# Kernel optimization log

Hardware: AMD Instinct MI355X
Metric: run time of the kernel (lower is better)

Reference implementation:

```python
import jax, jax.numpy as jnp
import numpy as np
import math

B, S, D = 4, 4096, 1024
H, HD, LK = 16, 64, 256


def setup_inputs() -> dict:
    key = jax.random.key(0)
    ks = jax.random.split(key, 8)
    s = 1.0 / math.sqrt(D)
    return {
        "X": jax.random.normal(ks[0], (B, S, D), jnp.float32),
        "mask": jnp.ones((B, S), jnp.float32),
        "Wq": jax.random.normal(ks[1], (D, H * HD), jnp.float32) * s,
        "bq": jnp.zeros((H * HD,), jnp.float32),
        "Wk": jax.random.normal(ks[2], (D, H * HD), jnp.float32) * s,
        "bk": jnp.zeros((H * HD,), jnp.float32),
        "Wv": jax.random.normal(ks[3], (D, H * HD), jnp.float32) * s,
        "bv": jnp.zeros((H * HD,), jnp.float32),
        "E": jax.random.normal(ks[4], (H, LK, S), jnp.float32) / math.sqrt(LK),
        "Wo": jax.random.normal(ks[5], (H * HD, D), jnp.float32) * s,
        "bo": jnp.zeros((D,), jnp.float32),
    }


def reference(X, mask, Wq, bq, Wk, bk, Wv, bv, E, Wo, bo):
    Bd, Sd, Dd = X.shape

    def split_heads(t):  # [B,S,H*HD] -> [B,H,S,HD]
        return t.reshape(Bd, Sd, H, HD).transpose(0, 2, 1, 3)

    Q = split_heads(X @ Wq + bq)
    K = split_heads(X @ Wk + bk)
    V = split_heads(X @ Wv + bv)

    m = mask[:, None, :, None]  # [B,1,S,1]
    # Low-rank projection along sequence: [H,LK,S] x [B,H,S,HD] -> [B,H,LK,HD]
    Kp = jnp.einsum('hks,bhsd->bhkd', E, K * m)
    Vp = jnp.einsum('hks,bhsd->bhkd', E, V * m)

    dot = jnp.einsum('bhsd,bhkd->bhsk', Q, Kp) / math.sqrt(HD)
    attn = jax.nn.softmax(dot, axis=-1)
    Xo = jnp.einsum('bhsk,bhkd->bhsd', attn, Vp)

    Xo = Xo.transpose(0, 2, 1, 3).reshape(Bd, Sd, H * HD)
    return Xo @ Wo + bo
```

## Files before the change

kernel.cpp:

```cpp
#include <hip/hip_runtime.h>
#include <hip/hip_bf16.h>
#include <stdint.h>

typedef __bf16 bf16_t;
typedef __attribute__((ext_vector_type(8))) __bf16 bf16x8;
typedef __attribute__((ext_vector_type(4))) __bf16 bf16x4;
typedef __attribute__((ext_vector_type(4))) float f32x4;

#define TO_GLB(p) ((const __attribute__((address_space(1))) void*)(p))
#define TO_LDS(p) ((__attribute__((address_space(3))) void*)(p))

__global__ __launch_bounds__(256) void cast_bf16_kernel(const float* __restrict__ src,
                                                        bf16_t* __restrict__ dst, int n4) {
  int i = blockIdx.x * 256 + threadIdx.x;
  if (i < n4) {
    float4 v = ((const float4*)src)[i];
    bf16x4 o;
    o[0] = (bf16_t)v.x; o[1] = (bf16_t)v.y; o[2] = (bf16_t)v.z; o[3] = (bf16_t)v.w;
    ((bf16x4*)dst)[i] = o;
  }
}

__global__ __launch_bounds__(256) void transpose_cast(const float* __restrict__ W,
                                                      bf16_t* __restrict__ out, int R, int C) {
  __shared__ bf16_t tile[64][72];
  int r0 = blockIdx.y * 64, c0 = blockIdx.x * 64;
  int tid = threadIdx.x;
#pragma unroll
  for (int p = 0; p < 4; ++p) {
    int r = p * 16 + (tid >> 4);
    int c = (tid & 15) * 4;
    float4 v = *(const float4*)(W + (size_t)(r0 + r) * C + c0 + c);
    tile[r][c + 0] = (bf16_t)v.x; tile[r][c + 1] = (bf16_t)v.y;
    tile[r][c + 2] = (bf16_t)v.z; tile[r][c + 3] = (bf16_t)v.w;
  }
  __syncthreads();
#pragma unroll
  for (int p = 0; p < 4; ++p) {
    int c = p * 16 + (tid >> 4);
    int r = (tid & 15) * 4;
    bf16x4 o;
    o[0] = tile[r + 0][c]; o[1] = tile[r + 1][c];
    o[2] = tile[r + 2][c]; o[3] = tile[r + 3][c];
    *(bf16x4*)(out + (size_t)(c0 + c) * R + r0 + r) = o;
  }
}

__global__ __launch_bounds__(256) void gemm_bt_128(
    const bf16_t* __restrict__ A, const bf16_t* __restrict__ B, int K, int mode,
    const float* __restrict__ bq, const float* __restrict__ bk, const float* __restrict__ bv,
    const float* __restrict__ mask,
    bf16_t* __restrict__ Q, bf16_t* __restrict__ KT, bf16_t* __restrict__ VT,
    const float* __restrict__ bo, float* __restrict__ out) {
  int tid = threadIdx.x;
  int lane = tid & 63, wv = tid >> 6;
  int wm = wv >> 1, wn = wv & 1;
  int q = lane >> 4, m_in = lane & 15;
  size_t m0 = (size_t)blockIdx.x * 128;
  size_t n0 = (size_t)blockIdx.y * 128;
  const bf16_t* Ab = A + m0 * K;
  const bf16_t* Bb = B + n0 * K;
  __shared__ __align__(16) bf16_t As[128 * 32];
  __shared__ __align__(16) bf16_t Bs[128 * 32];

  f32x4 acc[4][4];
  f32x4 z = {0.f, 0.f, 0.f, 0.f};
#pragma unroll
  for (int mt = 0; mt < 4; ++mt)
#pragma unroll
    for (int nt = 0; nt < 4; ++nt) acc[mt][nt] = z;

  for (int k0 = 0; k0 < K; k0 += 32) {
#pragma unroll
    for (int i = 0; i < 2; ++i) {
      int ch = wv * 128 + i * 64 + lane;
      const bf16_t* ga = Ab + (size_t)(ch >> 2) * K + k0 + (ch & 3) * 8;
      __builtin_amdgcn_global_load_lds(TO_GLB(ga), TO_LDS(As + (wv * 2 + i) * 512), 16, 0, 0);
      const bf16_t* gb = Bb + (size_t)(ch >> 2) * K + k0 + (ch & 3) * 8;
      __builtin_amdgcn_global_load_lds(TO_GLB(gb), TO_LDS(Bs + (wv * 2 + i) * 512), 16, 0, 0);
    }
    __syncthreads();
    bf16x8 af[4], bfr[4];
#pragma unroll
    for (int t = 0; t < 4; ++t)
      af[t] = *(const bf16x8*)(As + (wm * 64 + t * 16 + m_in) * 32 + q * 8);
#pragma unroll
    for (int t = 0; t < 4; ++t)
      bfr[t] = *(const bf16x8*)(Bs + (wn * 64 + t * 16 + m_in) * 32 + q * 8);
#pragma unroll
    for (int mt = 0; mt < 4; ++mt)
#pragma unroll
      for (int nt = 0; nt < 4; ++nt)
        acc[mt][nt] = __builtin_amdgcn_mfma_f32_16x16x32_bf16(af[mt], bfr[nt], acc[mt][nt], 0, 0, 0);
    __syncthreads();
  }

  if (mode == 0) {
#pragma unroll
    for (int mt = 0; mt < 4; ++mt) {
      int mbase = (int)m0 + wm * 64 + mt * 16 + q * 4;
      int b = mbase >> 12, s = mbase & 4095;
      float mk[4];
#pragma unroll
      for (int r = 0; r < 4; ++r) mk[r] = mask[b * 4096 + s + r];
#pragma unroll
      for (int nt = 0; nt < 4; ++nt) {
        int nG = (int)n0 + wn * 64 + nt * 16 + m_in;
        int proj = nG >> 10, c = nG & 1023, h = c >> 6, hd = c & 63;
        const float* bp = (proj == 0) ? bq : ((proj == 1) ? bk : bv);
        float bias = bp[c];
        if (proj == 0) {
#pragma unroll
          for (int r = 0; r < 4; ++r)
            Q[((size_t)(b * 16 + h) * 4096 + s + r) * 64 + hd] = (bf16_t)(acc[mt][nt][r] + bias);
        } else {
          bf16_t* dst = (proj == 1) ? KT : VT;
          bf16x4 v;
#pragma unroll
          for (int r = 0; r < 4; ++r) v[r] = (bf16_t)((acc[mt][nt][r] + bias) * mk[r]);
          *(bf16x4*)(dst + ((size_t)(b * 16 + h) * 64 + hd) * 4096 + s) = v;
        }
      }
    }
  } else {
#pragma unroll
    for (int mt = 0; mt < 4; ++mt) {
      int t = (int)m0 + wm * 64 + mt * 16 + q * 4;
#pragma unroll
      for (int nt = 0; nt < 4; ++nt) {
        int nG = (int)n0 + wn * 64 + nt * 16 + m_in;
        float bias = bo[nG];
#pragma unroll
        for (int r = 0; r < 4; ++r) out[(size_t)(t + r) * 1024 + nG] = acc[mt][nt][r] + bias;
      }
    }
  }
}

__global__ __launch_bounds__(512) void gemm2_kernel(
    const bf16_t* __restrict__ E, const bf16_t* __restrict__ KT, const bf16_t* __restrict__ VT,
    bf16_t* __restrict__ Kp, bf16_t* __restrict__ VpT) {
  int tid = threadIdx.x, lane = tid & 63, wv = tid >> 6;
  int wm = wv >> 1, wn = wv & 1;
  int q = lane >> 4, m_in = lane & 15;
  int mt0 = blockIdx.x;
  int bh = blockIdx.y;
  int kv = blockIdx.z;
  int h = bh & 15;
  const bf16_t* Ab = E + (size_t)h * 256 * 4096 + (size_t)mt0 * 128 * 4096;
  const bf16_t* Bb = (kv ? VT : KT) + (size_t)bh * 64 * 4096;
  __shared__ __align__(16) bf16_t As[4 * 128 * 32];
  __shared__ __align__(16) bf16_t Bs[4 * 64 * 32];

  f32x4 acc[2][2];
  f32x4 z = {0.f, 0.f, 0.f, 0.f};
#pragma unroll
  for (int mt = 0; mt < 2; ++mt)
#pragma unroll
    for (int nt = 0; nt < 2; ++nt) acc[mt][nt] = z;

  for (int k0 = 0; k0 < 4096; k0 += 128) {
#pragma unroll
    for (int it = 0; it < 4; ++it) {
      int l = it * 512 + tid;
      int sub = l >> 9, row = (l >> 2) & 127, cc = l & 3;
      const bf16_t* ga = Ab + (size_t)row * 4096 + k0 + sub * 32 + cc * 8;
      __builtin_amdgcn_global_load_lds(TO_GLB(ga), TO_LDS(As + (it * 512 + wv * 64) * 8), 16, 0, 0);
    }
#pragma unroll
    for (int it = 0; it < 2; ++it) {
      int l = it * 512 + tid;
      int sub = l >> 8, row = (l >> 2) & 63, cc = l & 3;
      const bf16_t* gb = Bb + (size_t)row * 4096 + k0 + sub * 32 + cc * 8;
      __builtin_amdgcn_global_load_lds(TO_GLB(gb), TO_LDS(Bs + (it * 512 + wv * 64) * 8), 16, 0, 0);
    }
    __syncthreads();
#pragma unroll
    for (int kk = 0; kk < 4; ++kk) {
      bf16x8 af[2], bfr[2];
#pragma unroll
      for (int mt = 0; mt < 2; ++mt)
        af[mt] = *(const bf16x8*)(As + kk * 4096 + (wm * 32 + mt * 16 + m_in) * 32 + q * 8);
#pragma unroll
      for (int nt = 0; nt < 2; ++nt)
        bfr[nt] = *(const bf16x8*)(Bs + kk * 2048 + (wn * 32 + nt * 16 + m_in) * 32 + q * 8);
#pragma unroll
      for (int mt = 0; mt < 2; ++mt)
#pragma unroll
        for (int nt = 0; nt < 2; ++nt)
          acc[mt][nt] = __builtin_amdgcn_mfma_f32_16x16x32_bf16(af[mt], bfr[nt], acc[mt][nt], 0, 0, 0);
    }
    __syncthreads();
  }

#pragma unroll
  for (int mt = 0; mt < 2; ++mt) {
    int lk = mt0 * 128 + wm * 32 + mt * 16 + q * 4;
#pragma unroll
    for (int nt = 0; nt < 2; ++nt) {
      int hd = wn * 32 + nt * 16 + m_in;
      if (kv == 0) {
#pragma unroll
        for (int r = 0; r < 4; ++r)
          Kp[(size_t)bh * 16384 + (size_t)(lk + r) * 64 + hd] = (bf16_t)acc[mt][nt][r];
      } else {
        bf16x4 v;
#pragma unroll
        for (int r = 0; r < 4; ++r) v[r] = (bf16_t)acc[mt][nt][r];
        *(bf16x4*)(VpT + (size_t)bh * 16384 + (size_t)hd * 256 + lk) = v;
      }
    }
  }
}

__global__ __launch_bounds__(256) void attn_kernel(
    const bf16_t* __restrict__ Q, const bf16_t* __restrict__ Kp, const bf16_t* __restrict__ VpT,
    bf16_t* __restrict__ Xo) {
  int tid = threadIdx.x, lane = tid & 63, wv = tid >> 6;
  int q = lane >> 4, m_in = lane & 15;
  int s0 = blockIdx.x * 64;
  int bh = blockIdx.y;
  int b = bh >> 4, h = bh & 15;
  const bf16_t* Qb = Q + ((size_t)bh * 4096 + s0 + wv * 16) * 64;
  const bf16_t* Kpb = Kp + (size_t)bh * 16384;
  const bf16_t* Vb = VpT + (size_t)bh * 16384;
  __shared__ __align__(16) bf16_t buf[16384];

#pragma unroll
  for (int it = 0; it < 8; ++it) {
    int l = it * 256 + tid;
    int sub = l >> 10, row = (l >> 2) & 255, cc = l & 3;
    const bf16_t* g = Kpb + row * 64 + sub * 32 + cc * 8;
    __builtin_amdgcn_global_load_lds(TO_GLB(g), TO_LDS(buf + (it * 256 + wv * 64) * 8), 16, 0, 0);
  }
  bf16x8 aq[2];
#pragma unroll
  for (int ks = 0; ks < 2; ++ks) aq[ks] = *(const bf16x8*)(Qb + (size_t)m_in * 64 + ks * 32 + q * 8);
  __syncthreads();

  f32x4 sc[16];
  f32x4 z = {0.f, 0.f, 0.f, 0.f};
#pragma unroll
  for (int nt = 0; nt < 16; ++nt) sc[nt] = z;
#pragma unroll
  for (int nt = 0; nt < 16; ++nt)
#pragma unroll
    for (int ks = 0; ks < 2; ++ks) {
      bf16x8 kb = *(const bf16x8*)(buf + ks * 8192 + (nt * 16 + m_in) * 32 + q * 8);
      sc[nt] = __builtin_amdgcn_mfma_f32_16x16x32_bf16(aq[ks], kb, sc[nt], 0, 0, 0);
    }

  float mx[4], sm[4];
#pragma unroll
  for (int r = 0; r < 4; ++r) mx[r] = -1e30f;
#pragma unroll
  for (int nt = 0; nt < 16; ++nt)
#pragma unroll
    for (int r = 0; r < 4; ++r) {
      float t = sc[nt][r] * 0.125f;
      sc[nt][r] = t;
      mx[r] = fmaxf(mx[r], t);
    }
#pragma unroll
  for (int off = 1; off < 16; off <<= 1)
#pragma unroll
    for (int r = 0; r < 4; ++r) mx[r] = fmaxf(mx[r], __shfl_xor(mx[r], off));
#pragma unroll
  for (int r = 0; r < 4; ++r) sm[r] = 0.f;
#pragma unroll
  for (int nt = 0; nt < 16; ++nt)
#pragma unroll
    for (int r = 0; r < 4; ++r) {
      float e = __expf(sc[nt][r] - mx[r]);
      sc[nt][r] = e;
      sm[r] += e;
    }
#pragma unroll
  for (int off = 1; off < 16; off <<= 1)
#pragma unroll
    for (int r = 0; r < 4; ++r) sm[r] += __shfl_xor(sm[r], off);
  float inv[4];
#pragma unroll
  for (int r = 0; r < 4; ++r) inv[r] = 1.0f / sm[r];

  __syncthreads();

  bf16_t* Pw = buf + wv * 4096;
#pragma unroll
  for (int nt = 0; nt < 16; ++nt) {
    int cw = nt * 2 + (m_in >> 3);
#pragma unroll
    for (int r = 0; r < 4; ++r) {
      int rp = q * 4 + r;
      int sw = (((cw ^ (rp & 7)) << 3) | (m_in & 7));
      Pw[rp * 256 + sw] = (bf16_t)(sc[nt][r] * inv[r]);
    }
  }
  bf16x8 pa[8];
#pragma unroll
  for (int ks = 0; ks < 8; ++ks) {
    int c = ks * 4 + q;
    pa[ks] = *(const bf16x8*)(Pw + m_in * 256 + ((c ^ (m_in & 7)) << 3));
  }
  __syncthreads();

#pragma unroll
  for (int it = 0; it < 8; ++it) {
    int l = it * 256 + tid;
    int sub = l >> 8, row = (l >> 2) & 63, cc = l & 3;
    const bf16_t* g = Vb + row * 256 + sub * 32 + cc * 8;
    __builtin_amdgcn_global_load_lds(TO_GLB(g), TO_LDS(buf + (it * 256 + wv * 64) * 8), 16, 0, 0);
  }
  __syncthreads();

  f32x4 o[4];
#pragma unroll
  for (int nt = 0; nt < 4; ++nt) o[nt] = z;
#pragma unroll
  for (int nt = 0; nt < 4; ++nt)
#pragma unroll
    for (int ks = 0; ks < 8; ++ks) {
      bf16x8 vb = *(const bf16x8*)(buf + ks * 2048 + (nt * 16 + m_in) * 32 + q * 8);
      o[nt] = __builtin_amdgcn_mfma_f32_16x16x32_bf16(pa[ks], vb, o[nt], 0, 0, 0);
    }

#pragma unroll
  for (int nt = 0; nt < 4; ++nt)
#pragma unroll
    for (int r = 0; r < 4; ++r)
      Xo[((size_t)b * 4096 + s0 + wv * 16 + q * 4 + r) * 1024 + h * 64 + nt * 16 + m_in] =
          (bf16_t)o[nt][r];
}

extern "C" void kernel_launch(void* const* d_in, const int* in_sizes, int n_in,
                              void* d_out, int out_size, void* d_ws, size_t ws_size,
                              hipStream_t stream) {
  const float* X = (const float*)d_in[0];
  const float* mask = (const float*)d_in[1];
  const float* Wq = (const float*)d_in[2];
  const float* bq = (const float*)d_in[3];
  const float* Wk = (const float*)d_in[4];
  const float* bk = (const float*)d_in[5];
  const float* Wv = (const float*)d_in[6];
  const float* bv = (const float*)d_in[7];
  const float* E = (const float*)d_in[8];
  const float* Wo = (const float*)d_in[9];
  const float* bo = (const float*)d_in[10];
  float* out = (float*)d_out;

  char* ws = (char*)d_ws;
  const size_t SZ = 33554432;
  bf16_t* Xb = (bf16_t*)(ws);
  bf16_t* Eb = (bf16_t*)(ws + SZ);
  bf16_t* Qb = (bf16_t*)(ws + 2 * SZ);
  bf16_t* KT = (bf16_t*)(ws + 3 * SZ);
  bf16_t* VT = (bf16_t*)(ws + 4 * SZ);
  bf16_t* Kp = (bf16_t*)(ws + 5 * SZ);
  bf16_t* VpT = (bf16_t*)(ws + 5 * SZ + 8388608);
  bf16_t* WqkvT = (bf16_t*)(ws + 5 * SZ + 2 * 8388608);
  bf16_t* WoT = (bf16_t*)(ws + 5 * SZ + 2 * 8388608 + 6291456);
  bf16_t* Xo = Xb;

  cast_bf16_kernel<<<16384, 256, 0, stream>>>(X, Xb, 4194304);
  cast_bf16_kernel<<<16384, 256, 0, stream>>>(E, Eb, 4194304);
  dim3 tg(16, 16);
  transpose_cast<<<tg, 256, 0, stream>>>(Wq, WqkvT, 1024, 1024);
  transpose_cast<<<tg, 256, 0, stream>>>(Wk, WqkvT + 1048576, 1024, 1024);
  transpose_cast<<<tg, 256, 0, stream>>>(Wv, WqkvT + 2097152, 1024, 1024);
  transpose_cast<<<tg, 256, 0, stream>>>(Wo, WoT, 1024, 1024);

  gemm_bt_128<<<dim3(128, 24), 256, 0, stream>>>(Xb, WqkvT, 1024, 0, bq, bk, bv, mask,
                                                 Qb, KT, VT, nullptr, nullptr);
  gemm2_kernel<<<dim3(2, 64, 2), 512, 0, stream>>>(Eb, KT, VT, Kp, VpT);
  attn_kernel<<<dim3(64, 64), 256, 0, stream>>>(Qb, Kp, VpT, Xo);
  gemm_bt_128<<<dim3(128, 8), 256, 0, stream>>>(Xo, WoT, 1024, 1, nullptr, nullptr, nullptr,
                                                nullptr, nullptr, nullptr, nullptr, bo, out);
}
```

Measured before the change: 521.5 us.

## Widen GEMM K-tile to 64 with XOR-swizzled LDS and batch prep kernels

The bf16 GEMM now stages 64-wide K slices per iteration instead of 32. This halves the barrier and loop overhead per K and doubles the MFMA work between syncs. The LDS layout is XOR-swizzled on 16-byte chunks to avoid bank conflicts on the fragment reads. Separately, the two cast launches and the four weight-transpose launches are merged into one launch each to cut launch overhead. LDS use doubles to 32KB per block, which may reduce occupancy.

```diff
diff --git a/kernel.cpp b/kernel.cpp
--- a/kernel.cpp
+++ b/kernel.cpp
@@ -10,27 +10,36 @@
 #define TO_GLB(p) ((const __attribute__((address_space(1))) void*)(p))
 #define TO_LDS(p) ((__attribute__((address_space(3))) void*)(p))
 
-__global__ __launch_bounds__(256) void cast_bf16_kernel(const float* __restrict__ src,
-                                                        bf16_t* __restrict__ dst, int n4) {
+__global__ __launch_bounds__(256) void cast2_bf16_kernel(const float* __restrict__ a,
+                                                         bf16_t* __restrict__ da,
+                                                         const float* __restrict__ b,
+                                                         bf16_t* __restrict__ db, int n4) {
   int i = blockIdx.x * 256 + threadIdx.x;
-  if (i < n4) {
-    float4 v = ((const float4*)src)[i];
-    bf16x4 o;
-    o[0] = (bf16_t)v.x; o[1] = (bf16_t)v.y; o[2] = (bf16_t)v.z; o[3] = (bf16_t)v.w;
-    ((bf16x4*)dst)[i] = o;
-  }
-}
-
-__global__ __launch_bounds__(256) void transpose_cast(const float* __restrict__ W,
-                                                      bf16_t* __restrict__ out, int R, int C) {
+  const float* s = (i < n4) ? a : b;
+  bf16_t* d = (i < n4) ? da : db;
+  int j = (i < n4) ? i : i - n4;
+  float4 v = ((const float4*)s)[j];
+  bf16x4 o;
+  o[0] = (bf16_t)v.x; o[1] = (bf16_t)v.y; o[2] = (bf16_t)v.z; o[3] = (bf16_t)v.w;
+  ((bf16x4*)d)[j] = o;
+}
+
+__global__ __launch_bounds__(256) void transpose_cast4(
+    const float* __restrict__ W0, const float* __restrict__ W1, const float* __restrict__ W2,
+    const float* __restrict__ W3, bf16_t* __restrict__ o0, bf16_t* __restrict__ o1,
+    bf16_t* __restrict__ o2, bf16_t* __restrict__ o3) {
+  const int RC = 1024;
   __shared__ bf16_t tile[64][72];
+  int z = blockIdx.z;
+  const float* W = (z == 0) ? W0 : (z == 1) ? W1 : (z == 2) ? W2 : W3;
+  bf16_t* out = (z == 0) ? o0 : (z == 1) ? o1 : (z == 2) ? o2 : o3;
   int r0 = blockIdx.y * 64, c0 = blockIdx.x * 64;
   int tid = threadIdx.x;
 #pragma unroll
   for (int p = 0; p < 4; ++p) {
     int r = p * 16 + (tid >> 4);
     int c = (tid & 15) * 4;
-    float4 v = *(const float4*)(W + (size_t)(r0 + r) * C + c0 + c);
+    float4 v = *(const float4*)(W + (size_t)(r0 + r) * RC + c0 + c);
     tile[r][c + 0] = (bf16_t)v.x; tile[r][c + 1] = (bf16_t)v.y;
     tile[r][c + 2] = (bf16_t)v.z; tile[r][c + 3] = (bf16_t)v.w;
   }
@@ -42,7 +51,7 @@
     bf16x4 o;
     o[0] = tile[r + 0][c]; o[1] = tile[r + 1][c];
     o[2] = tile[r + 2][c]; o[3] = tile[r + 3][c];
-    *(bf16x4*)(out + (size_t)(c0 + c) * R + r0 + r) = o;
+    *(bf16x4*)(out + (size_t)(c0 + c) * RC + r0 + r) = o;
   }
 }
 
@@ -60,8 +69,8 @@
   size_t n0 = (size_t)blockIdx.y * 128;
   const bf16_t* Ab = A + m0 * K;
   const bf16_t* Bb = B + n0 * K;
-  __shared__ __align__(16) bf16_t As[128 * 32];
-  __shared__ __align__(16) bf16_t Bs[128 * 32];
+  __shared__ __align__(16) bf16_t As[128 * 64];
+  __shared__ __align__(16) bf16_t Bs[128 * 64];
 
   f32x4 acc[4][4];
   f32x4 z = {0.f, 0.f, 0.f, 0.f};
@@ -70,28 +79,34 @@
 #pragma unroll
     for (int nt = 0; nt < 4; ++nt) acc[mt][nt] = z;
 
-  for (int k0 = 0; k0 < K; k0 += 32) {
-#pragma unroll
-    for (int i = 0; i < 2; ++i) {
-      int ch = wv * 128 + i * 64 + lane;
-      const bf16_t* ga = Ab + (size_t)(ch >> 2) * K + k0 + (ch & 3) * 8;
-      __builtin_amdgcn_global_load_lds(TO_GLB(ga), TO_LDS(As + (wv * 2 + i) * 512), 16, 0, 0);
-      const bf16_t* gb = Bb + (size_t)(ch >> 2) * K + k0 + (ch & 3) * 8;
-      __builtin_amdgcn_global_load_lds(TO_GLB(gb), TO_LDS(Bs + (wv * 2 + i) * 512), 16, 0, 0);
+  for (int k0 = 0; k0 < K; k0 += 64) {
+#pragma unroll
+    for (int it = 0; it < 4; ++it) {
+      int l = it * 256 + tid;
+      int row = l >> 3, cc = l & 7;
+      int gcc = cc ^ (row & 7);
+      const bf16_t* ga = Ab + (size_t)row * K + k0 + gcc * 8;
+      __builtin_amdgcn_global_load_lds(TO_GLB(ga), TO_LDS(As + (it * 256 + wv * 64) * 8), 16, 0, 0);
+      const bf16_t* gb = Bb + (size_t)row * K + k0 + gcc * 8;
+      __builtin_amdgcn_global_load_lds(TO_GLB(gb), TO_LDS(Bs + (it * 256 + wv * 64) * 8), 16, 0, 0);
     }
     __syncthreads();
-    bf16x8 af[4], bfr[4];
-#pragma unroll
-    for (int t = 0; t < 4; ++t)
-      af[t] = *(const bf16x8*)(As + (wm * 64 + t * 16 + m_in) * 32 + q * 8);
-#pragma unroll
-    for (int t = 0; t < 4; ++t)
-      bfr[t] = *(const bf16x8*)(Bs + (wn * 64 + t * 16 + m_in) * 32 + q * 8);
-#pragma unroll
-    for (int mt = 0; mt < 4; ++mt)
-#pragma unroll
-      for (int nt = 0; nt < 4; ++nt)
-        acc[mt][nt] = __builtin_amdgcn_mfma_f32_16x16x32_bf16(af[mt], bfr[nt], acc[mt][nt], 0, 0, 0);
+#pragma unroll
+    for (int kk = 0; kk < 2; ++kk) {
+      bf16x8 af[4], bfr[4];
+#pragma unroll
+      for (int t = 0; t < 4; ++t) {
+        int ra = wm * 64 + t * 16 + m_in;
+        af[t] = *(const bf16x8*)(As + ra * 64 + (((kk * 4 + q) ^ (ra & 7)) * 8));
+        int rb = wn * 64 + t * 16 + m_in;
+        bfr[t] = *(const bf16x8*)(Bs + rb * 64 + (((kk * 4 + q) ^ (rb & 7)) * 8));
+      }
+#pragma unroll
+      for (int mt = 0; mt < 4; ++mt)
+#pragma unroll
+        for (int nt = 0; nt < 4; ++nt)
+          acc[mt][nt] = __builtin_amdgcn_mfma_f32_16x16x32_bf16(af[mt], bfr[nt], acc[mt][nt], 0, 0, 0);
+    }
     __syncthreads();
   }
 
@@ -361,13 +376,9 @@
   bf16_t* WoT = (bf16_t*)(ws + 5 * SZ + 2 * 8388608 + 6291456);
   bf16_t* Xo = Xb;
 
-  cast_bf16_kernel<<<16384, 256, 0, stream>>>(X, Xb, 4194304);
-  cast_bf16_kernel<<<16384, 256, 0, stream>>>(E, Eb, 4194304);
-  dim3 tg(16, 16);
-  transpose_cast<<<tg, 256, 0, stream>>>(Wq, WqkvT, 1024, 1024);
-  transpose_cast<<<tg, 256, 0, stream>>>(Wk, WqkvT + 1048576, 1024, 1024);
-  transpose_cast<<<tg, 256, 0, stream>>>(Wv, WqkvT + 2097152, 1024, 1024);
-  transpose_cast<<<tg, 256, 0, stream>>>(Wo, WoT, 1024, 1024);
+  cast2_bf16_kernel<<<32768, 256, 0, stream>>>(X, Xb, E, Eb, 4194304);
+  transpose_cast4<<<dim3(16, 16, 4), 256, 0, stream>>>(
+      Wq, Wk, Wv, Wo, WqkvT, WqkvT + 1048576, WqkvT + 2097152, WoT);
 
   gemm_bt_128<<<dim3(128, 24), 256, 0, stream>>>(Xb, WqkvT, 1024, 0, bq, bk, bv, mask,
                                                  Qb, KT, VT, nullptr, nullptr);
```

New measurement: 471.7 us. 1.11x faster.
